# Optimization experiments

Measured on AMD Instinct MI355X. Metric: run time of the kernel, lower is better.

The kernel has to match this reference:

```python
import jax, jax.numpy as jnp
import numpy as np

B, T, N, D = 32, 12, 325, 64
H = 4           # geo_num_heads == t_num_heads
HD = D // H     # head_dim = 16
M_SP = 32       # spatial frequency modes (min(32, N//2))
M_T = T // 2    # temporal frequency modes (all low modes)
SCALE = HD ** -0.5


def _lin(x, W):
    # torch nn.Linear (no bias): y = x @ W.T, W: [out, in]
    return jnp.einsum('btnd,ed->btne', x, W)


def _spatial(x, Wq, Wk, Wv, weights_Q, sp_modes):
    # FEDformer-style frequency attention over the node axis N
    q, k, v = _lin(x, Wq), _lin(x, Wk), _lin(x, Wv)          # [B,T,N,D]
    prep = lambda y: y.reshape(B, T, N, H, HD).transpose(0, 1, 3, 4, 2)  # [B,T,H,HD,N]
    qn = prep(q) / jnp.linalg.norm(q)   # global Frobenius norm (torch.norm with no dim)
    kn = prep(k) / jnp.linalg.norm(k)
    vn = prep(v)
    # rfft over nodes, gather selected modes (scatter-into-zeros in torch == gather here
    # since target indices are 0..M-1)
    qf = jnp.fft.rfft(qn, axis=-1)[..., sp_modes]            # [B,T,H,HD,M] c64
    kf = jnp.fft.rfft(kn, axis=-1)[..., sp_modes]
    vf = jnp.fft.rfft(vn, axis=-1)[..., sp_modes]
    M = M_SP
    qg = qf.transpose(0, 1, 2, 4, 3)[:, :, :, :, None, :]    # [B,T,H,M,1,HD]
    wq = jnp.broadcast_to(weights_Q.astype(jnp.complex64), (B, T, H, M, M - 1, HD))
    q_cat = jnp.concatenate([qg, wq], axis=4)                # [B,T,H,M,M,HD]
    kg = kf.transpose(0, 1, 2, 4, 3)[:, :, :, None, :, :]    # [B,T,H,1,M,HD]
    att = kg * jnp.conj(q_cat) * SCALE                       # [B,T,H,M,M,HD] c64
    att = jax.nn.softmax(jnp.abs(att), axis=-2).astype(jnp.complex64)
    att = att.transpose(0, 1, 2, 3, 5, 4)                    # [B,T,H,M,HD,M]
    vg = vf[:, :, :, None, :, :]                             # [B,T,H,1,HD,M]
    out = (vg * jnp.conj(att)).mean(axis=3)                  # [B,T,H,HD,M]
    out_ft = jnp.zeros((B, T, H, HD, N // 2 + 1), jnp.complex64).at[..., sp_modes].set(out)
    y = jnp.fft.irfft(out_ft, n=N, axis=-1)                  # [B,T,H,HD,N]
    return y.transpose(0, 1, 4, 2, 3).reshape(B, T, N, D)


def _temporal(x, Wq, Wk, Wv, weights_Q_t, t_modes):
    # frequency attention over the time axis T with causal (tril) mask.
    # NOTE: torch reshapes the [B,T,N,D] buffer directly as [B,N,T,H,HD] (raw view),
    # so we replicate that exact buffer reinterpretation.
    q, k, v = _lin(x, Wq), _lin(x, Wk), _lin(x, Wv)
    prep = lambda y: y.reshape(B, N, T, H, HD).transpose(0, 1, 3, 4, 2)  # [B,N,H,HD,T]
    qn = prep(q); kn = prep(k); vn = prep(v)
    qn = qn / jnp.linalg.norm(qn)
    kn = kn / jnp.linalg.norm(kn)
    qf = jnp.fft.rfft(qn, axis=-1)[..., t_modes]             # [B,N,H,HD,Mt]
    kf = jnp.fft.rfft(kn, axis=-1)[..., t_modes]
    vf = jnp.fft.rfft(vn, axis=-1)[..., t_modes]
    Mt = M_T
    qg = qf.transpose(0, 1, 2, 4, 3)[:, :, :, :, None, :]    # [B,N,H,Mt,1,HD]
    wq = jnp.broadcast_to(weights_Q_t.astype(jnp.complex64), (B, N, H, Mt, Mt - 1, HD))
    q_cat = jnp.concatenate([qg, wq], axis=4)                # [B,N,H,Mt,Mt,HD]
    kg = kf.transpose(0, 1, 2, 4, 3)[:, :, :, :, None, :]    # [B,N,H,Mt,1,HD] (unsqueeze(4) in torch)
    att = kg * jnp.conj(q_cat) * SCALE                       # [B,N,H,Mt,Mt,HD]
    att = att.transpose(0, 1, 2, 5, 3, 4)                    # [B,N,H,HD,Mt,Mt]
    mask = jnp.tril(jnp.ones((Mt, Mt), jnp.float32))
    att = att * mask                                         # zero above diagonal
    attw = jax.nn.softmax(jnp.abs(att), axis=-1).astype(jnp.complex64)
    vg = vf[..., None]                                       # [B,N,H,HD,Mt,1]
    out = (vg * jnp.conj(attw)).mean(axis=-1)                # [B,N,H,HD,Mt]
    out_ft = jnp.zeros((B, N, H, HD, T // 2 + 1), jnp.complex64).at[..., t_modes].set(out)
    y = jnp.fft.irfft(out_ft, n=T, axis=-1)                  # [B,N,H,HD,T]
    return y.transpose(0, 4, 1, 2, 3).reshape(B, T, N, D)


def _gcn(x, adj, W_fc1, W_mlp, b_mlp):
    a = adj / jnp.sum(adj, axis=1, keepdims=True)            # row-normalized
    agg = jnp.einsum('btkd,nk->btnd', x, a)
    h = jnp.einsum('btnd,ed->btne', agg, W_fc1)              # fc1 (no bias)
    return jnp.einsum('btnd,ed->btne', h, W_mlp) + b_mlp     # mlp (bias)


def _forward(x, adj, Wq_geo, Wk_geo, Wv_geo, Wq_t, Wk_t, Wv_t,
             W_fc1, W_mlp, b_mlp, weights_Q, weights_Q_t, sp_modes, t_modes):
    gcn_out = _gcn(x, adj, W_fc1, W_mlp, b_mlp)
    sp_x = _spatial(x, Wq_geo, Wk_geo, Wv_geo, weights_Q, sp_modes)
    te_x = _temporal(x, Wq_t, Wk_t, Wv_t, weights_Q_t, t_modes)
    return gcn_out + sp_x + te_x   # proj_drop is identity (p=0)


def setup_inputs() -> dict:
    key = jax.random.key(0)
    ks = jax.random.split(key, 13)
    w = lambda k, s: jax.random.normal(k, s, dtype=jnp.float32) * 0.05
    rng = np.random.default_rng(0)
    sp_modes = np.sort(rng.permutation(N // 2)[:M_SP]).astype(np.int32)
    t_modes = np.arange(M_T, dtype=np.int32)  # modes_T == T//2 selects all low modes
    return {
        'x': jax.random.normal(ks[0], (B, T, N, D), dtype=jnp.float32),
        'adj': jax.random.uniform(ks[1], (N, N), dtype=jnp.float32),
        'Wq_geo': w(ks[2], (D, D)), 'Wk_geo': w(ks[3], (D, D)), 'Wv_geo': w(ks[4], (D, D)),
        'Wq_t': w(ks[5], (D, D)), 'Wk_t': w(ks[6], (D, D)), 'Wv_t': w(ks[7], (D, D)),
        'W_fc1': w(ks[8], (D, D)), 'W_mlp': w(ks[9], (D, D)), 'b_mlp': w(ks[10], (D,)),
        'weights_Q': jax.random.normal(ks[11], (M_SP, M_SP - 1, HD), dtype=jnp.float32),
        'weights_Q_t': jax.random.normal(ks[12], (M_T, M_T - 1, HD), dtype=jnp.float32),
        'sp_modes': jnp.asarray(sp_modes),
        't_modes': jnp.asarray(t_modes),
    }


def reference(x, adj, Wq_geo, Wk_geo, Wv_geo, Wq_t, Wk_t, Wv_t,
              W_fc1, W_mlp, b_mlp, weights_Q, weights_Q_t, sp_modes, t_modes):
    return _forward(x, adj, Wq_geo, Wk_geo, Wv_geo, Wq_t, Wk_t, Wv_t,
                    W_fc1, W_mlp, b_mlp, weights_Q, weights_Q_t, sp_modes, t_modes)
```

## Files before the change

### kernel.cpp

```cpp
#include <hip/hip_runtime.h>


typedef unsigned short u16;
typedef short short8 __attribute__((ext_vector_type(8)));
typedef float floatx4 __attribute__((ext_vector_type(4)));

__device__ __forceinline__ u16 f2bf(float f) {
  union { float fp; unsigned int u; } v; v.fp = f;
  unsigned int x = v.u;
  x += 0x7FFF + ((x >> 16) & 1);
  return (u16)(x >> 16);
}

constexpr size_t OFF_NORM = 4096;
constexpr size_t OFF_WQA  = 8208;
constexpr size_t OFF_ANB  = 24080;
constexpr size_t OFF_TB   = 81280;
constexpr size_t OFF_T2   = 102080;
constexpr size_t OFF_OFT  = 112480;
constexpr size_t OFF_XCT  = 898912;
constexpr size_t OFF_VT   = 5224288;
constexpr size_t OFF_ALT  = 13211488;
constexpr size_t OFF_WBB  = OFF_ALT;
constexpr size_t OFF_WSPB = OFF_ALT + 8192;

__global__ __launch_bounds__(256) void k_prep(const float* __restrict__ adj,
                                              const float* __restrict__ Wmlp,
                                              const float* __restrict__ Wfc1,
                                              const float* __restrict__ wQ,
                                              const float* __restrict__ Wvt,
                                              const float* __restrict__ Wq,
                                              const float* __restrict__ Wk,
                                              const float* __restrict__ Wv,
                                              const int* __restrict__ sp_modes,
                                              float* __restrict__ ws) {
  __shared__ float red[256];
  const int tid = threadIdx.x;
  const int blk = blockIdx.x;
  u16* WBBu = (u16*)(ws + OFF_WBB);
  if (blk == 0) {
    for (int o = tid; o < 4096; o += 256) {
      int g = o >> 6, dd = o & 63;
      float s = 0.f;
      for (int e = 0; e < 64; ++e)
        s = fmaf(Wmlp[g * 64 + e], Wfc1[e * 64 + dd], s);
      WBBu[o] = f2bf(s);
    }
  } else if (blk < 9) {
    for (int i = (blk - 1) * 256 + tid; i < 15872; i += 2048)
      ws[OFF_WQA + i] = fabsf(wQ[i]);
  } else if (blk < 334) {
    const int n = blk - 9;
    float p = 0.f;
    for (int k = tid; k < 325; k += 256) p += adj[n * 325 + k];
    red[tid] = p;
    __syncthreads();
    for (int s2 = 128; s2 > 0; s2 >>= 1) {
      if (tid < s2) red[tid] += red[tid + s2];
      __syncthreads();
    }
    const float inv = 1.f / red[0];
    u16* ANB = (u16*)(ws + OFF_ANB);
    for (int k = tid; k < 352; k += 256)
      ANB[(size_t)n * 352 + k] = (k < 325) ? f2bf(adj[n * 325 + k] * inv) : (u16)0;
  } else if (blk < 366) {
    const int j = blk - 334;
    const int f = sp_modes[j];
    const float wgt = (f == 0) ? 1.f : 2.f;
    u16* T2B = (u16*)(ws + OFF_T2);
    u16* TB = (u16*)(ws + OFF_TB);
    const int row_re = 8 * (j >> 2) + (j & 3);
    const int row_im = row_re + 4;
    for (int n = tid; n < 352; n += 256) {
      float c = 0.f, s = 0.f;
      if (n < 325) {
        int mm = (f * n) % 325;
        float th = 6.283185307179586f * (float)mm * (1.f / 325.f);
        c = cosf(th);
        s = sinf(th);
      }
      TB[(size_t)row_re * 352 + n] = f2bf(c);
      TB[(size_t)row_im * 352 + n] = f2bf(-s);
      if (n < 325) {
        T2B[(size_t)n * 64 + 2 * j] = f2bf(wgt * (1.f / 325.f) * c);
        T2B[(size_t)n * 64 + 2 * j + 1] = f2bf(-wgt * (1.f / 325.f) * s);
      }
    }
  } else if (blk == 366) {
    for (int i = tid; i < 12288; i += 256) {
      const int r = i >> 6, e = i & 63;
      const float* src = (r < 64) ? Wvt : (r < 128) ? Wq : Wk;
      WBBu[4096 + i] = f2bf(src[(size_t)(r & 63) * 64 + e]);
    }
  } else if (blk == 367) {
    u16* WSPBu = (u16*)(ws + OFF_WSPB);
    for (int i = tid; i < 12288; i += 256) {
      const int r = i >> 6, e = i & 63;
      const float* src = (r < 64) ? Wq : (r < 128) ? Wk : Wv;
      WSPBu[i] = f2bf(src[(size_t)(r & 63) * 64 + e]);
    }
  } else {
    const int idx = (blk - 368) * 256 + tid;
    u16* p = (u16*)(ws + OFF_XCT) + (size_t)(idx >> 6) * 22528 + (size_t)(idx & 63) * 352;
    for (int c = 325; c < 352; ++c) p[c] = 0;
  }
}

__global__ __launch_bounds__(512, 3) void k_linear2(const float* __restrict__ x,
                                                    float* __restrict__ ws) {
  __shared__ __align__(16) u16 XA[128 * 72];
  __shared__ float reds[16];
  const int tid = threadIdx.x;
  const int wv = tid >> 6, lane = tid & 63, lc = lane & 15, quad = lane >> 4;
  const size_t base = (size_t)blockIdx.x * 128;
  const u16* WBBu = (const u16*)(ws + OFF_WBB);

  for (int i = tid; i < 2048; i += 512) {
    const int row = i >> 4, e0 = (i & 15) * 4;
    const float4 v = *(const float4*)(x + (base + row) * 64 + e0);
    u16* dst = &XA[row * 72 + e0];
    dst[0] = f2bf(v.x); dst[1] = f2bf(v.y); dst[2] = f2bf(v.z); dst[3] = f2bf(v.w);
  }
  __syncthreads();

  floatx4 acc[16] = {};
#pragma unroll
  for (int kc = 0; kc < 2; ++kc) {
    const short8 af = *(const short8*)&XA[(16 * wv + lc) * 72 + kc * 32 + quad * 8];
#pragma unroll
    for (int ni = 0; ni < 16; ++ni) {
      const short8 bf_ = *(const short8*)&WBBu[(ni * 16 + lc) * 64 + kc * 32 + quad * 8];
      acc[ni] = __builtin_amdgcn_mfma_f32_16x16x32_bf16(af, bf_, acc[ni], 0, 0, 0);
    }
  }

  float sq = 0.f, sk = 0.f;
#pragma unroll
  for (int reg = 0; reg < 4; ++reg) {
    const int row = 16 * wv + quad * 4 + reg;
#pragma unroll
    for (int ni = 0; ni < 4; ++ni)
      ws[OFF_VT + (base + row) * 64 + ni * 16 + lc] = acc[4 + ni][reg];
#pragma unroll
    for (int ni = 0; ni < 4; ++ni) {
      const float v = acc[8 + ni][reg];
      sq = fmaf(v, v, sq);
    }
#pragma unroll
    for (int ni = 0; ni < 4; ++ni) {
      const float v = acc[12 + ni][reg];
      sk = fmaf(v, v, sk);
    }
  }
  for (int off = 32; off > 0; off >>= 1) {
    sq += __shfl_down(sq, off);
    sk += __shfl_down(sk, off);
  }
  if (lane == 0) { reds[wv] = sq; reds[8 + wv] = sk; }
  __syncthreads();
  if (tid == 0)
    atomicAdd(&ws[OFF_NORM + 0], reds[0] + reds[1] + reds[2] + reds[3] +
                                 reds[4] + reds[5] + reds[6] + reds[7]);
  if (tid == 1)
    atomicAdd(&ws[OFF_NORM + 1], reds[8] + reds[9] + reds[10] + reds[11] +
                                 reds[12] + reds[13] + reds[14] + reds[15]);

  u16* xcT = XA;
#pragma unroll
  for (int ni = 0; ni < 4; ++ni)
#pragma unroll
    for (int reg = 0; reg < 4; ++reg)
      xcT[(ni * 16 + lc) * 132 + 16 * wv + quad * 4 + reg] = f2bf(acc[ni][reg]);
  __syncthreads();
  u16* XCT = (u16*)(ws + OFF_XCT);
  for (int i = tid; i < 8192; i += 512) {
    const int d = i >> 7, r = i & 127;
    const unsigned int row = (unsigned int)(base + r);
    const unsigned int bt = row / 325u;
    const unsigned int n = row - bt * 325u;
    XCT[(size_t)bt * 22528 + (size_t)d * 352 + n] = xcT[d * 132 + r];
  }
}

__global__ __launch_bounds__(256) void k_spatial3(const float* __restrict__ x,
                                                  float* __restrict__ ws) {
  __shared__ __align__(16) float smem[10240];
  const int tid = threadIdx.x;
  const int bt = blockIdx.x;
  const int lane = tid & 63, wv = tid >> 6;
  const int lc = lane & 15, quad = lane >> 4;

  u16* Bt = (u16*)smem;
  u16* xfl2 = (u16*)smem + 5120;
  const u16* TB = (const u16*)(ws + OFF_TB);
  const u16* WSPBu = (const u16*)(ws + OFF_WSPB);
  const float* xb = x + (size_t)bt * 20800;
  const int br = tid & 31, be0 = (tid >> 5) * 8;

  auto stageB = [&](int kc, u16* dst) {
    const int k0 = kc * 32;
    float v[8];
    if (k0 + br < 325) {
      const float* src = xb + (size_t)(k0 + br) * 64 + be0;
      *(float4*)v = *(const float4*)src;
      *(float4*)(v + 4) = *(const float4*)(src + 4);
    } else {
#pragma unroll
      for (int u = 0; u < 8; ++u) v[u] = 0.f;
    }
#pragma unroll
    for (int u = 0; u < 8; ++u) dst[(be0 + u) * 40 + br] = f2bf(v[u]);
  };

  floatx4 accA[4] = {};
  stageB(0, Bt);
  __syncthreads();
  for (int kc = 0; kc < 11; ++kc) {
    u16* cur = Bt + (kc & 1) * 2560;
    if (kc < 10) stageB(kc + 1, Bt + ((kc + 1) & 1) * 2560);
    const short8 af = *(const short8*)&TB[(size_t)(16 * wv + lc) * 352 + kc * 32 + quad * 8];
#pragma unroll
    for (int t = 0; t < 4; ++t) {
      const short8 bf_ = *(const short8*)&cur[(t * 16 + lc) * 40 + quad * 8];
      accA[t] = __builtin_amdgcn_mfma_f32_16x16x32_bf16(af, bf_, accA[t], 0, 0, 0);
    }
    __syncthreads();
  }

#pragma unroll
  for (int t = 0; t < 4; ++t)
#pragma unroll
    for (int r = 0; r < 4; ++r)
      xfl2[(t >> 1) * 2560 + (16 * wv + quad * 4 + r) * 40 + (t & 1) * 16 + lc] =
          f2bf(accA[t][r]);
  __syncthreads();

  floatx4 acc2[12] = {};
#pragma unroll
  for (int kc2 = 0; kc2 < 2; ++kc2) {
    const short8 af2 = *(const short8*)&xfl2[kc2 * 2560 + (16 * wv + lc) * 40 + quad * 8];
#pragma unroll
    for (int t = 0; t < 12; ++t) {
      const short8 bf2 = *(const short8*)&WSPBu[(t * 16 + lc) * 64 + kc2 * 32 + quad * 8];
      acc2[t] = __builtin_amdgcn_mfma_f32_16x16x32_bf16(af2, bf2, acc2[t], 0, 0, 0);
    }
  }
  __syncthreads();

  float* sq_q = smem;
  float* sq_k = smem + 2048;
  float* vfre = smem + 4096;
  float* vfim = smem + 6144;
  float* wbar = smem + 8192;
  for (int i = tid; i < 2048; i += 256) wbar[i] = 0.f;
  {
    const int fb = 8 * wv + ((quad >= 2) ? 4 : 0);
    const int isim = quad & 1;
#pragma unroll
    for (int t = 0; t < 12; ++t) {
      const int mat = t >> 2;
      const int d = (t & 3) * 16 + lc;
#pragma unroll
      for (int r = 0; r < 4; ++r) {
        const float v = acc2[t][r];
        if (mat == 2) {
          if (isim) vfim[(fb + r) * 64 + d] = v;
          else vfre[(fb + r) * 64 + d] = v;
        } else {
          const float s2 = v * v + __shfl_xor(v * v, 16);
          if (!isim) {
            if (mat == 0) sq_q[(fb + r) * 64 + d] = s2;
            else sq_k[(fb + r) * 64 + d] = s2;
          }
        }
      }
    }
  }
  __syncthreads();
  const float inv_nq = rsqrtf(ws[OFF_NORM + 0]);
  const float inv_nk = rsqrtf(ws[OFF_NORM + 1]);
  for (int i = tid; i < 2048; i += 256)
    sq_k[i] = 0.25f * inv_nk * sqrtf(sq_k[i]);
  __syncthreads();
  {
    const int d = tid & 63, fb2 = tid >> 6, hd = d & 15;
    const float* wqa = ws + OFF_WQA;
    float wacc[32];
#pragma unroll
    for (int j = 0; j < 32; ++j) wacc[j] = 0.f;
    for (int r8 = 0; r8 < 8; ++r8) {
      const int m = fb2 + (r8 << 2);
      const float aq = inv_nq * sqrtf(sq_q[m * 64 + d]);
      float sv[32];
      float mx = -1e30f;
#pragma unroll
      for (int j = 0; j < 32; ++j) {
        const float a = (j == 0) ? aq : wqa[(m * 31 + (j - 1)) * 16 + hd];
        const float s = sq_k[j * 64 + d] * a;
        sv[j] = s;
        mx = fmaxf(mx, s);
      }
      float sum = 0.f;
#pragma unroll
      for (int j = 0; j < 32; ++j) {
        const float ev = __expf(sv[j] - mx);
        sv[j] = ev;
        sum += ev;
      }
      const float sc = 0.03125f / sum;
#pragma unroll
      for (int j = 0; j < 32; ++j) wacc[j] += sv[j] * sc;
    }
#pragma unroll
    for (int j = 0; j < 32; ++j) atomicAdd(&wbar[j * 64 + d], wacc[j]);
  }
  __syncthreads();
  unsigned int* OFTu = (unsigned int*)(ws + OFF_OFT) + (size_t)bt * 2048;
  for (int i2 = tid; i2 < 2048; i2 += 256) {
    const int d = i2 >> 5, j = i2 & 31;
    const float w = wbar[j * 64 + d];
    const unsigned int lo = f2bf(vfre[j * 64 + d] * w);
    const unsigned int hi = f2bf(vfim[j * 64 + d] * w);
    OFTu[i2] = lo | (hi << 16);
  }
}

__global__ __launch_bounds__(256) void k_alt(float* __restrict__ ws) {
  const int idx = blockIdx.x * 256 + threadIdx.x;
  if (idx >= 32 * 325 * 64) return;
  const int dd = idx & 63;
  const int n = (idx >> 6) % 325;
  const int b = idx / (64 * 325);
  const float* vt = ws + OFF_VT + ((size_t)b * 3900 + (size_t)n * 12) * 64 + dd;
  float s = 0.f, sign = 1.f;
  for (int k = 0; k < 12; ++k) {
    s += sign * vt[k * 64];
    sign = -sign;
  }
  ws[OFF_ALT + idx] = s;
}

__global__ __launch_bounds__(256) void k_final2(const float* __restrict__ bmlp,
                                                float* __restrict__ ws,
                                                float* __restrict__ out) {
  const int tid = threadIdx.x;
  const int bt = blockIdx.x / 3, mc = blockIdx.x % 3;
  const int m0 = mc * 128;
  const int wave = tid >> 6, lane = tid & 63;
  const int quad = lane >> 4, lc = lane & 15;

  const u16* ANB = (const u16*)(ws + OFF_ANB);
  const u16* T2B = (const u16*)(ws + OFF_T2);
  const u16* XCT = (const u16*)(ws + OFF_XCT) + (size_t)bt * 22528;
  const u16* OFT = (const u16*)(ws + OFF_OFT) + (size_t)bt * 4096;

  floatx4 acc[2][4] = {};

#pragma unroll
  for (int c13 = 0; c13 < 13; ++c13) {
    const bool gcn = (c13 < 11);
    const u16* Asrc = gcn ? ANB : T2B;
    const int astr = gcn ? 352 : 64;
    const int acol = gcn ? c13 * 32 : (c13 - 11) * 32;
    const u16* Bsrc = gcn ? XCT : OFT;
    const int bstr = gcn ? 352 : 64;
    short8 af[2], bf_[4];
#pragma unroll
    for (int mi = 0; mi < 2; ++mi) {
      const int gr = m0 + wave * 32 + mi * 16 + lc;
      short8 a = {};
      if (gr < 325)
        a = *(const short8*)&Asrc[(size_t)gr * astr + acol + quad * 8];
      af[mi] = a;
    }
#pragma unroll
    for (int ni = 0; ni < 4; ++ni)
      bf_[ni] = *(const short8*)&Bsrc[(size_t)(ni * 16 + lc) * bstr + acol + quad * 8];
#pragma unroll
    for (int mi = 0; mi < 2; ++mi)
#pragma unroll
      for (int ni = 0; ni < 4; ++ni)
        acc[mi][ni] = __builtin_amdgcn_mfma_f32_16x16x32_bf16(
            af[mi], bf_[ni], acc[mi][ni], 0, 0, 0);
  }

  const int b = bt / 12, t = bt - b * 12;
  const float sgn = (t & 1) ? -1.f : 1.f;
#pragma unroll
  for (int ni = 0; ni < 4; ++ni) {
    const int d = ni * 16 + lc;
    const float bias = bmlp[d];
#pragma unroll
    for (int mi = 0; mi < 2; ++mi) {
#pragma unroll
      for (int reg = 0; reg < 4; ++reg) {
        const int n = m0 + wave * 32 + mi * 16 + quad * 4 + reg;
        if (n >= 325) continue;
        const float v = ws[OFF_VT + ((size_t)b * 3900 + (size_t)n * 12 + t) * 64 + d];
        const float al = ws[OFF_ALT + ((size_t)b * 325 + n) * 64 + d];
        const float te = (v - sgn * al * (1.f / 12.f)) * (1.f / 6.f);
        out[((size_t)bt * 325 + n) * 64 + d] = acc[mi][ni][reg] + bias + te;
      }
    }
  }
}

extern "C" void kernel_launch(void* const* d_in, const int* in_sizes, int n_in,
                              void* d_out, int out_size, void* d_ws, size_t ws_size,
                              hipStream_t stream) {
  const float* x = (const float*)d_in[0];
  const float* adj = (const float*)d_in[1];
  const float* Wq_g = (const float*)d_in[2];
  const float* Wk_g = (const float*)d_in[3];
  const float* Wv_g = (const float*)d_in[4];
  const float* Wv_t = (const float*)d_in[7];
  const float* Wfc1 = (const float*)d_in[8];
  const float* Wmlp = (const float*)d_in[9];
  const float* bmlp = (const float*)d_in[10];
  const float* wQ = (const float*)d_in[11];
  const int* sp_modes = (const int*)d_in[13];
  float* ws = (float*)d_ws;
  float* out = (float*)d_out;

  (void)in_sizes; (void)n_in; (void)out_size; (void)ws_size;

  hipMemsetAsync(ws + OFF_NORM, 0, 2 * sizeof(float), stream);
  k_prep<<<464, 256, 0, stream>>>(adj, Wmlp, Wfc1, wQ, Wv_t, Wq_g, Wk_g, Wv_g,
                                  sp_modes, ws);
  k_linear2<<<975, 512, 0, stream>>>(x, ws);
  k_spatial3<<<384, 256, 0, stream>>>(x, ws);
  k_alt<<<2600, 256, 0, stream>>>(ws);
  k_final2<<<1152, 256, 0, stream>>>(bmlp, ws, out);
}
```

Before: 278.5 us.

## Replace norm atomics with per-block partials; double k_spatial3 threads to 512

k_linear2 now writes per-block partial sums of squares into a workspace array instead of issuing global float atomics. Every k_spatial3 block re-reduces those 975 partials, which also removes the memset launch. k_spatial3 moves to 512 threads: two wave groups split the MFMA N-tiles and the softmax rows, and duplicated wbar buffers are summed at the end. This adds parallelism per block (384 blocks on a large GPU) at the cost of redundant partial reduction in every block and more shared memory.

```diff
diff --git a/kernel.cpp b/kernel.cpp
--- a/kernel.cpp
+++ b/kernel.cpp
@@ -12,7 +12,7 @@
   return (u16)(x >> 16);
 }
 
-constexpr size_t OFF_NORM = 4096;
+constexpr size_t OFF_NPART = 4096;
 constexpr size_t OFF_WQA  = 8208;
 constexpr size_t OFF_ANB  = 24080;
 constexpr size_t OFF_TB   = 81280;
@@ -158,12 +158,13 @@
   }
   if (lane == 0) { reds[wv] = sq; reds[8 + wv] = sk; }
   __syncthreads();
-  if (tid == 0)
-    atomicAdd(&ws[OFF_NORM + 0], reds[0] + reds[1] + reds[2] + reds[3] +
-                                 reds[4] + reds[5] + reds[6] + reds[7]);
-  if (tid == 1)
-    atomicAdd(&ws[OFF_NORM + 1], reds[8] + reds[9] + reds[10] + reds[11] +
-                                 reds[12] + reds[13] + reds[14] + reds[15]);
+  if (tid == 0) {
+    const float a = reds[0] + reds[1] + reds[2] + reds[3] +
+                    reds[4] + reds[5] + reds[6] + reds[7];
+    const float b = reds[8] + reds[9] + reds[10] + reds[11] +
+                    reds[12] + reds[13] + reds[14] + reds[15];
+    *(float2*)(ws + OFF_NPART + 2 * (size_t)blockIdx.x) = make_float2(a, b);
+  }
 
   u16* xcT = XA;
 #pragma unroll
@@ -182,67 +183,84 @@
   }
 }
 
-__global__ __launch_bounds__(256) void k_spatial3(const float* __restrict__ x,
+__global__ __launch_bounds__(512) void k_spatial3(const float* __restrict__ x,
                                                   float* __restrict__ ws) {
-  __shared__ __align__(16) float smem[10240];
+  __shared__ __align__(16) float smem[12544];
   const int tid = threadIdx.x;
   const int bt = blockIdx.x;
   const int lane = tid & 63, wv = tid >> 6;
   const int lc = lane & 15, quad = lane >> 4;
+  const int wg = wv & 3;
+  const int wh = wv >> 2;
+
+  {
+    float psq = 0.f, psk = 0.f;
+    for (int p = tid; p < 975; p += 512) {
+      const float2 v = *(const float2*)(ws + OFF_NPART + 2 * (size_t)p);
+      psq += v.x; psk += v.y;
+    }
+    for (int off = 32; off > 0; off >>= 1) {
+      psq += __shfl_down(psq, off);
+      psk += __shfl_down(psk, off);
+    }
+    if (lane == 0) { smem[12480 + wv] = psq; smem[12488 + wv] = psk; }
+  }
 
   u16* Bt = (u16*)smem;
   u16* xfl2 = (u16*)smem + 5120;
   const u16* TB = (const u16*)(ws + OFF_TB);
   const u16* WSPBu = (const u16*)(ws + OFF_WSPB);
   const float* xb = x + (size_t)bt * 20800;
-  const int br = tid & 31, be0 = (tid >> 5) * 8;
+  const int br = tid & 31, beg = (tid >> 5) * 4;
 
   auto stageB = [&](int kc, u16* dst) {
     const int k0 = kc * 32;
-    float v[8];
+    float v[4];
     if (k0 + br < 325) {
-      const float* src = xb + (size_t)(k0 + br) * 64 + be0;
-      *(float4*)v = *(const float4*)src;
-      *(float4*)(v + 4) = *(const float4*)(src + 4);
+      *(float4*)v = *(const float4*)(xb + (size_t)(k0 + br) * 64 + beg);
     } else {
 #pragma unroll
-      for (int u = 0; u < 8; ++u) v[u] = 0.f;
-    }
-#pragma unroll
-    for (int u = 0; u < 8; ++u) dst[(be0 + u) * 40 + br] = f2bf(v[u]);
+      for (int u = 0; u < 4; ++u) v[u] = 0.f;
+    }
+#pragma unroll
+    for (int u = 0; u < 4; ++u) dst[(beg + u) * 40 + br] = f2bf(v[u]);
   };
 
-  floatx4 accA[4] = {};
+  floatx4 accA[2] = {};
   stageB(0, Bt);
   __syncthreads();
   for (int kc = 0; kc < 11; ++kc) {
     u16* cur = Bt + (kc & 1) * 2560;
     if (kc < 10) stageB(kc + 1, Bt + ((kc + 1) & 1) * 2560);
-    const short8 af = *(const short8*)&TB[(size_t)(16 * wv + lc) * 352 + kc * 32 + quad * 8];
-#pragma unroll
-    for (int t = 0; t < 4; ++t) {
+    const short8 af = *(const short8*)&TB[(size_t)(16 * wg + lc) * 352 + kc * 32 + quad * 8];
+#pragma unroll
+    for (int ti = 0; ti < 2; ++ti) {
+      const int t = wh * 2 + ti;
       const short8 bf_ = *(const short8*)&cur[(t * 16 + lc) * 40 + quad * 8];
-      accA[t] = __builtin_amdgcn_mfma_f32_16x16x32_bf16(af, bf_, accA[t], 0, 0, 0);
+      accA[ti] = __builtin_amdgcn_mfma_f32_16x16x32_bf16(af, bf_, accA[ti], 0, 0, 0);
     }
     __syncthreads();
   }
 
 #pragma unroll
-  for (int t = 0; t < 4; ++t)
+  for (int ti = 0; ti < 2; ++ti) {
+    const int t = wh * 2 + ti;
 #pragma unroll
     for (int r = 0; r < 4; ++r)
-      xfl2[(t >> 1) * 2560 + (16 * wv + quad * 4 + r) * 40 + (t & 1) * 16 + lc] =
-          f2bf(accA[t][r]);
-  __syncthreads();
-
-  floatx4 acc2[12] = {};
+      xfl2[wh * 2560 + (16 * wg + quad * 4 + r) * 40 + ti * 16 + lc] =
+          f2bf(accA[ti][r]);
+  }
+  __syncthreads();
+
+  floatx4 acc2[6] = {};
 #pragma unroll
   for (int kc2 = 0; kc2 < 2; ++kc2) {
-    const short8 af2 = *(const short8*)&xfl2[kc2 * 2560 + (16 * wv + lc) * 40 + quad * 8];
-#pragma unroll
-    for (int t = 0; t < 12; ++t) {
+    const short8 af2 = *(const short8*)&xfl2[kc2 * 2560 + (16 * wg + lc) * 40 + quad * 8];
+#pragma unroll
+    for (int tt = 0; tt < 6; ++tt) {
+      const int t = wh * 6 + tt;
       const short8 bf2 = *(const short8*)&WSPBu[(t * 16 + lc) * 64 + kc2 * 32 + quad * 8];
-      acc2[t] = __builtin_amdgcn_mfma_f32_16x16x32_bf16(af2, bf2, acc2[t], 0, 0, 0);
+      acc2[tt] = __builtin_amdgcn_mfma_f32_16x16x32_bf16(af2, bf2, acc2[tt], 0, 0, 0);
     }
   }
   __syncthreads();
@@ -252,17 +270,18 @@
   float* vfre = smem + 4096;
   float* vfim = smem + 6144;
   float* wbar = smem + 8192;
-  for (int i = tid; i < 2048; i += 256) wbar[i] = 0.f;
+  for (int i = tid; i < 4096; i += 512) wbar[i] = 0.f;
   {
-    const int fb = 8 * wv + ((quad >= 2) ? 4 : 0);
+    const int fb = 8 * wg + ((quad >= 2) ? 4 : 0);
     const int isim = quad & 1;
 #pragma unroll
-    for (int t = 0; t < 12; ++t) {
+    for (int tt = 0; tt < 6; ++tt) {
+      const int t = wh * 6 + tt;
       const int mat = t >> 2;
       const int d = (t & 3) * 16 + lc;
 #pragma unroll
       for (int r = 0; r < 4; ++r) {
-        const float v = acc2[t][r];
+        const float v = acc2[tt][r];
         if (mat == 2) {
           if (isim) vfim[(fb + r) * 64 + d] = v;
           else vfre[(fb + r) * 64 + d] = v;
@@ -277,19 +296,23 @@
     }
   }
   __syncthreads();
-  const float inv_nq = rsqrtf(ws[OFF_NORM + 0]);
-  const float inv_nk = rsqrtf(ws[OFF_NORM + 1]);
-  for (int i = tid; i < 2048; i += 256)
+  float nqs = 0.f, nks = 0.f;
+#pragma unroll
+  for (int w = 0; w < 8; ++w) { nqs += smem[12480 + w]; nks += smem[12488 + w]; }
+  const float inv_nq = rsqrtf(nqs);
+  const float inv_nk = rsqrtf(nks);
+  for (int i = tid; i < 2048; i += 512)
     sq_k[i] = 0.25f * inv_nk * sqrtf(sq_k[i]);
   __syncthreads();
   {
-    const int d = tid & 63, fb2 = tid >> 6, hd = d & 15;
+    const int d = tid & 63, fb2 = (tid >> 6) & 7, hd = d & 15;
+    float* wbarH = wbar + (tid >> 8) * 2048;
     const float* wqa = ws + OFF_WQA;
     float wacc[32];
 #pragma unroll
     for (int j = 0; j < 32; ++j) wacc[j] = 0.f;
-    for (int r8 = 0; r8 < 8; ++r8) {
-      const int m = fb2 + (r8 << 2);
+    for (int r4 = 0; r4 < 4; ++r4) {
+      const int m = fb2 + (r4 << 3);
       const float aq = inv_nq * sqrtf(sq_q[m * 64 + d]);
       float sv[32];
       float mx = -1e30f;
@@ -312,13 +335,13 @@
       for (int j = 0; j < 32; ++j) wacc[j] += sv[j] * sc;
     }
 #pragma unroll
-    for (int j = 0; j < 32; ++j) atomicAdd(&wbar[j * 64 + d], wacc[j]);
+    for (int j = 0; j < 32; ++j) atomicAdd(&wbarH[j * 64 + d], wacc[j]);
   }
   __syncthreads();
   unsigned int* OFTu = (unsigned int*)(ws + OFF_OFT) + (size_t)bt * 2048;
-  for (int i2 = tid; i2 < 2048; i2 += 256) {
+  for (int i2 = tid; i2 < 2048; i2 += 512) {
     const int d = i2 >> 5, j = i2 & 31;
-    const float w = wbar[j * 64 + d];
+    const float w = wbar[j * 64 + d] + wbar[2048 + j * 64 + d];
     const unsigned int lo = f2bf(vfre[j * 64 + d] * w);
     const unsigned int hi = f2bf(vfim[j * 64 + d] * w);
     OFTu[i2] = lo | (hi << 16);
@@ -424,11 +447,10 @@
 
   (void)in_sizes; (void)n_in; (void)out_size; (void)ws_size;
 
-  hipMemsetAsync(ws + OFF_NORM, 0, 2 * sizeof(float), stream);
   k_prep<<<464, 256, 0, stream>>>(adj, Wmlp, Wfc1, wQ, Wv_t, Wq_g, Wk_g, Wv_g,
                                   sp_modes, ws);
   k_linear2<<<975, 512, 0, stream>>>(x, ws);
-  k_spatial3<<<384, 256, 0, stream>>>(x, ws);
+  k_spatial3<<<384, 512, 0, stream>>>(x, ws);
   k_alt<<<2600, 256, 0, stream>>>(ws);
   k_final2<<<1152, 256, 0, stream>>>(bmlp, ws, out);
 }
```

Result: slower. 301.1 us (+8.1%).

## Apply temporal value projection after alternating-sum reduction and drop norm atomics

Applied to the files above, without the earlier changes.

The temporal V projection is no longer computed for every token and stored as a large fp32 buffer. By linearity, the alternating-sign sum over time is taken on raw x (k_xa), and the combined (x - sgn*alt/12)/6 is projected with Wv_t inside the final MFMA kernel. This removes a sizeable fp32 write and two reads of it, at the cost of extra MFMAs and x reads in k_final2, plus bf16 rounding of the combined term. The global norm atomics and memset are also replaced by per-block partial sums that each spatial block reduces itself.

```diff
diff --git a/kernel.cpp b/kernel.cpp
--- a/kernel.cpp
+++ b/kernel.cpp
@@ -12,17 +12,17 @@
   return (u16)(x >> 16);
 }
 
-constexpr size_t OFF_NORM = 4096;
+constexpr size_t OFF_NPART = 4096;
 constexpr size_t OFF_WQA  = 8208;
 constexpr size_t OFF_ANB  = 24080;
 constexpr size_t OFF_TB   = 81280;
+constexpr size_t OFF_WVTB = 92544;
+constexpr size_t OFF_WBB  = 94592;
 constexpr size_t OFF_T2   = 102080;
 constexpr size_t OFF_OFT  = 112480;
 constexpr size_t OFF_XCT  = 898912;
-constexpr size_t OFF_VT   = 5224288;
-constexpr size_t OFF_ALT  = 13211488;
-constexpr size_t OFF_WBB  = OFF_ALT;
-constexpr size_t OFF_WSPB = OFF_ALT + 8192;
+constexpr size_t OFF_XA   = 13211488;
+constexpr size_t OFF_WSPB = OFF_XA + 8192;
 
 __global__ __launch_bounds__(256) void k_prep(const float* __restrict__ adj,
                                               const float* __restrict__ Wmlp,
@@ -87,9 +87,9 @@
       }
     }
   } else if (blk == 366) {
-    for (int i = tid; i < 12288; i += 256) {
+    for (int i = tid; i < 8192; i += 256) {
       const int r = i >> 6, e = i & 63;
-      const float* src = (r < 64) ? Wvt : (r < 128) ? Wq : Wk;
+      const float* src = (r < 64) ? Wq : Wk;
       WBBu[4096 + i] = f2bf(src[(size_t)(r & 63) * 64 + e]);
     }
   } else if (blk == 367) {
@@ -99,8 +99,11 @@
       const float* src = (r < 64) ? Wq : (r < 128) ? Wk : Wv;
       WSPBu[i] = f2bf(src[(size_t)(r & 63) * 64 + e]);
     }
+  } else if (blk == 368) {
+    u16* WVTBu = (u16*)(ws + OFF_WVTB);
+    for (int i = tid; i < 4096; i += 256) WVTBu[i] = f2bf(Wvt[i]);
   } else {
-    const int idx = (blk - 368) * 256 + tid;
+    const int idx = (blk - 369) * 256 + tid;
     u16* p = (u16*)(ws + OFF_XCT) + (size_t)(idx >> 6) * 22528 + (size_t)(idx & 63) * 352;
     for (int c = 325; c < 352; ++c) p[c] = 0;
   }
@@ -123,12 +126,12 @@
   }
   __syncthreads();
 
-  floatx4 acc[16] = {};
+  floatx4 acc[12] = {};
 #pragma unroll
   for (int kc = 0; kc < 2; ++kc) {
     const short8 af = *(const short8*)&XA[(16 * wv + lc) * 72 + kc * 32 + quad * 8];
 #pragma unroll
-    for (int ni = 0; ni < 16; ++ni) {
+    for (int ni = 0; ni < 12; ++ni) {
       const short8 bf_ = *(const short8*)&WBBu[(ni * 16 + lc) * 64 + kc * 32 + quad * 8];
       acc[ni] = __builtin_amdgcn_mfma_f32_16x16x32_bf16(af, bf_, acc[ni], 0, 0, 0);
     }
@@ -137,18 +140,14 @@
   float sq = 0.f, sk = 0.f;
 #pragma unroll
   for (int reg = 0; reg < 4; ++reg) {
-    const int row = 16 * wv + quad * 4 + reg;
-#pragma unroll
-    for (int ni = 0; ni < 4; ++ni)
-      ws[OFF_VT + (base + row) * 64 + ni * 16 + lc] = acc[4 + ni][reg];
+#pragma unroll
+    for (int ni = 0; ni < 4; ++ni) {
+      const float v = acc[4 + ni][reg];
+      sq = fmaf(v, v, sq);
+    }
 #pragma unroll
     for (int ni = 0; ni < 4; ++ni) {
       const float v = acc[8 + ni][reg];
-      sq = fmaf(v, v, sq);
-    }
-#pragma unroll
-    for (int ni = 0; ni < 4; ++ni) {
-      const float v = acc[12 + ni][reg];
       sk = fmaf(v, v, sk);
     }
   }
@@ -158,12 +157,13 @@
   }
   if (lane == 0) { reds[wv] = sq; reds[8 + wv] = sk; }
   __syncthreads();
-  if (tid == 0)
-    atomicAdd(&ws[OFF_NORM + 0], reds[0] + reds[1] + reds[2] + reds[3] +
-                                 reds[4] + reds[5] + reds[6] + reds[7]);
-  if (tid == 1)
-    atomicAdd(&ws[OFF_NORM + 1], reds[8] + reds[9] + reds[10] + reds[11] +
-                                 reds[12] + reds[13] + reds[14] + reds[15]);
+  if (tid == 0) {
+    const float a = reds[0] + reds[1] + reds[2] + reds[3] +
+                    reds[4] + reds[5] + reds[6] + reds[7];
+    const float b = reds[8] + reds[9] + reds[10] + reds[11] +
+                    reds[12] + reds[13] + reds[14] + reds[15];
+    *(float2*)(ws + OFF_NPART + 2 * (size_t)blockIdx.x) = make_float2(a, b);
+  }
 
   u16* xcT = XA;
 #pragma unroll
@@ -184,11 +184,24 @@
 
 __global__ __launch_bounds__(256) void k_spatial3(const float* __restrict__ x,
                                                   float* __restrict__ ws) {
-  __shared__ __align__(16) float smem[10240];
+  __shared__ __align__(16) float smem[10256];
   const int tid = threadIdx.x;
   const int bt = blockIdx.x;
   const int lane = tid & 63, wv = tid >> 6;
   const int lc = lane & 15, quad = lane >> 4;
+
+  {
+    float psq = 0.f, psk = 0.f;
+    for (int p = tid; p < 975; p += 256) {
+      const float2 v = *(const float2*)(ws + OFF_NPART + 2 * (size_t)p);
+      psq += v.x; psk += v.y;
+    }
+    for (int off = 32; off > 0; off >>= 1) {
+      psq += __shfl_down(psq, off);
+      psk += __shfl_down(psk, off);
+    }
+    if (lane == 0) { smem[10240 + wv] = psq; smem[10248 + wv] = psk; }
+  }
 
   u16* Bt = (u16*)smem;
   u16* xfl2 = (u16*)smem + 5120;
@@ -277,8 +290,11 @@
     }
   }
   __syncthreads();
-  const float inv_nq = rsqrtf(ws[OFF_NORM + 0]);
-  const float inv_nk = rsqrtf(ws[OFF_NORM + 1]);
+  float nqs = 0.f, nks = 0.f;
+#pragma unroll
+  for (int w = 0; w < 4; ++w) { nqs += smem[10240 + w]; nks += smem[10248 + w]; }
+  const float inv_nq = rsqrtf(nqs);
+  const float inv_nk = rsqrtf(nks);
   for (int i = tid; i < 2048; i += 256)
     sq_k[i] = 0.25f * inv_nk * sqrtf(sq_k[i]);
   __syncthreads();
@@ -325,22 +341,26 @@
   }
 }
 
-__global__ __launch_bounds__(256) void k_alt(float* __restrict__ ws) {
+__global__ __launch_bounds__(256) void k_xa(const float* __restrict__ x,
+                                            float* __restrict__ ws) {
   const int idx = blockIdx.x * 256 + threadIdx.x;
-  if (idx >= 32 * 325 * 64) return;
-  const int dd = idx & 63;
-  const int n = (idx >> 6) % 325;
-  const int b = idx / (64 * 325);
-  const float* vt = ws + OFF_VT + ((size_t)b * 3900 + (size_t)n * 12) * 64 + dd;
-  float s = 0.f, sign = 1.f;
+  if (idx >= 32 * 325 * 16) return;
+  const int dq = idx & 15;
+  const int n = (idx >> 4) % 325;
+  const int b = idx / (16 * 325);
+  const float* xp = x + ((size_t)b * 3900 + (size_t)n * 12) * 64 + dq * 4;
+  float4 s = make_float4(0.f, 0.f, 0.f, 0.f);
+  float sign = 1.f;
   for (int k = 0; k < 12; ++k) {
-    s += sign * vt[k * 64];
+    const float4 v = *(const float4*)(xp + (size_t)k * 64);
+    s.x += sign * v.x; s.y += sign * v.y; s.z += sign * v.z; s.w += sign * v.w;
     sign = -sign;
   }
-  ws[OFF_ALT + idx] = s;
-}
-
-__global__ __launch_bounds__(256) void k_final2(const float* __restrict__ bmlp,
+  *(float4*)(ws + OFF_XA + ((size_t)b * 325 + n) * 64 + dq * 4) = s;
+}
+
+__global__ __launch_bounds__(256) void k_final2(const float* __restrict__ x,
+                                                const float* __restrict__ bmlp,
                                                 float* __restrict__ ws,
                                                 float* __restrict__ out) {
   const int tid = threadIdx.x;
@@ -353,6 +373,10 @@
   const u16* T2B = (const u16*)(ws + OFF_T2);
   const u16* XCT = (const u16*)(ws + OFF_XCT) + (size_t)bt * 22528;
   const u16* OFT = (const u16*)(ws + OFF_OFT) + (size_t)bt * 4096;
+  const u16* WVTBu = (const u16*)(ws + OFF_WVTB);
+
+  const int b = bt / 12, t = bt - b * 12;
+  const float sgn12 = ((t & 1) ? -1.f : 1.f) * (1.f / 12.f);
 
   floatx4 acc[2][4] = {};
 
@@ -384,8 +408,38 @@
             af[mi], bf_[ni], acc[mi][ni], 0, 0, 0);
   }
 
-  const int b = bt / 12, t = bt - b * 12;
-  const float sgn = (t & 1) ? -1.f : 1.f;
+#pragma unroll
+  for (int kc = 0; kc < 2; ++kc) {
+    const int k0 = kc * 32 + quad * 8;
+    short8 af[2];
+#pragma unroll
+    for (int mi = 0; mi < 2; ++mi) {
+      const int nr = m0 + wave * 32 + mi * 16 + lc;
+      short8 a = {};
+      if (nr < 325) {
+        const float* xp = x + ((size_t)b * 3900 + (size_t)nr * 12 + t) * 64 + k0;
+        const float* xap = ws + OFF_XA + ((size_t)b * 325 + nr) * 64 + k0;
+        float xv[8], av[8];
+        *(float4*)xv = *(const float4*)xp;
+        *(float4*)(xv + 4) = *(const float4*)(xp + 4);
+        *(float4*)av = *(const float4*)xap;
+        *(float4*)(av + 4) = *(const float4*)(xap + 4);
+#pragma unroll
+        for (int u = 0; u < 8; ++u)
+          a[u] = (short)f2bf((xv[u] - sgn12 * av[u]) * (1.f / 6.f));
+      }
+      af[mi] = a;
+    }
+#pragma unroll
+    for (int ni = 0; ni < 4; ++ni) {
+      const short8 bf_ = *(const short8*)&WVTBu[(size_t)(ni * 16 + lc) * 64 + k0];
+#pragma unroll
+      for (int mi = 0; mi < 2; ++mi)
+        acc[mi][ni] = __builtin_amdgcn_mfma_f32_16x16x32_bf16(
+            af[mi], bf_, acc[mi][ni], 0, 0, 0);
+    }
+  }
+
 #pragma unroll
   for (int ni = 0; ni < 4; ++ni) {
     const int d = ni * 16 + lc;
@@ -396,10 +450,7 @@
       for (int reg = 0; reg < 4; ++reg) {
         const int n = m0 + wave * 32 + mi * 16 + quad * 4 + reg;
         if (n >= 325) continue;
-        const float v = ws[OFF_VT + ((size_t)b * 3900 + (size_t)n * 12 + t) * 64 + d];
-        const float al = ws[OFF_ALT + ((size_t)b * 325 + n) * 64 + d];
-        const float te = (v - sgn * al * (1.f / 12.f)) * (1.f / 6.f);
-        out[((size_t)bt * 325 + n) * 64 + d] = acc[mi][ni][reg] + bias + te;
+        out[((size_t)bt * 325 + n) * 64 + d] = acc[mi][ni][reg] + bias;
       }
     }
   }
@@ -424,11 +475,10 @@
 
   (void)in_sizes; (void)n_in; (void)out_size; (void)ws_size;
 
-  hipMemsetAsync(ws + OFF_NORM, 0, 2 * sizeof(float), stream);
-  k_prep<<<464, 256, 0, stream>>>(adj, Wmlp, Wfc1, wQ, Wv_t, Wq_g, Wk_g, Wv_g,
+  k_prep<<<465, 256, 0, stream>>>(adj, Wmlp, Wfc1, wQ, Wv_t, Wq_g, Wk_g, Wv_g,
                                   sp_modes, ws);
   k_linear2<<<975, 512, 0, stream>>>(x, ws);
   k_spatial3<<<384, 256, 0, stream>>>(x, ws);
-  k_alt<<<2600, 256, 0, stream>>>(ws);
-  k_final2<<<1152, 256, 0, stream>>>(bmlp, ws, out);
-}
+  k_xa<<<650, 256, 0, stream>>>(x, ws);
+  k_final2<<<1152, 256, 0, stream>>>(x, bmlp, ws, out);
+}
```

Result: faster. 255.2 us (-8.4%).
